# Kernel optimization log

Measured on AMD Instinct MI355X. Metric: run time of the kernel, lower is better.

Reference implementation:

```python
import jax, jax.numpy as jnp
import numpy as np

EPS = 1e-8  # matches torch F.cosine_similarity eps default


def setup_inputs() -> dict:
    key = jax.random.key(0)
    k1, k2 = jax.random.split(key)
    z = jax.random.normal(k1, (8192, 256), dtype=jnp.float32)            # [N, d] node latents
    embedding_weight = jax.random.normal(k2, (4096, 256), dtype=jnp.float32)  # [V, d] codebook
    return {"z": z, "embedding_weight": embedding_weight}


def _l2_normalize(x):
    # torch cosine_similarity clamps each norm at eps before dividing
    n = jnp.sqrt(jnp.sum(x * x, axis=-1, keepdims=True))
    return x / jnp.maximum(n, EPS)


def reference(z, embedding_weight):
    # decode_edges: sigmoid(z @ z^T) -> [N, N]
    adj = jax.nn.sigmoid(jnp.matmul(z, z.T))

    # decode_node_features: cosine similarity of every node latent vs every
    # codebook vector, then argmax over the codebook axis. Instead of the
    # naive [N, V, d] broadcast, normalize both sides and take a single
    # [N, d] x [d, V] matmul -> [N, V], then reduce with argmax.
    zn = _l2_normalize(z)                   # [N, d]
    en = _l2_normalize(embedding_weight)    # [V, d]
    cosine_sim = jnp.matmul(zn, en.T)       # [N, V]
    decoded_indices = jnp.argmax(cosine_sim, axis=1)  # [N] int

    return adj, decoded_indices
```

## Files before the change

kernel.cpp:

```cpp
#include <hip/hip_runtime.h>
#include <stdint.h>
#include <math.h>

#define D_DIM 256
#define NZ 8192
#define NV 4096
#define NBKT 256
#define THR_C 0.138f
#define MARGIN 0.012f

typedef __bf16 bf16;
typedef __attribute__((ext_vector_type(8))) __bf16 bf16x8;
typedef __attribute__((ext_vector_type(4))) float f32x4;

__device__ __forceinline__ void stage16(const bf16* g, bf16* lbase) {
#if __has_builtin(__builtin_amdgcn_global_load_lds)
  __builtin_amdgcn_global_load_lds(
      (const __attribute__((address_space(1))) void*)(uintptr_t)g,
      (__attribute__((address_space(3))) void*)(uint32_t)(uintptr_t)lbase,
      16, 0, 0);
#endif
}

__global__ void prep_kernel(const float* __restrict__ z, const float* __restrict__ E,
                            bf16* __restrict__ zh, bf16* __restrict__ zl,
                            bf16* __restrict__ eh, float* __restrict__ rinvZ,
                            float* __restrict__ rinvE,
                            unsigned long long* __restrict__ slots,
                            unsigned long long* __restrict__ cand) {
  __shared__ float red[4];
  const int row = blockIdx.x;
  const int t = threadIdx.x;
  const bool isZ = row < NZ;
  const int r = isZ ? row : row - NZ;
  const float* src = isZ ? z : E;
  const float x = src[(size_t)r * D_DIM + t];
  const bf16 h = (bf16)x;
  if (isZ) {
    zh[(size_t)r * D_DIM + t] = h;
    zl[(size_t)r * D_DIM + t] = (bf16)(x - (float)h);
    cand[(size_t)r * NBKT + t] = 0ull;
  } else {
    eh[(size_t)r * D_DIM + t] = h;
  }
  float s = x * x;
#pragma unroll
  for (int off = 32; off; off >>= 1) s += __shfl_xor(s, off);
  if ((t & 63) == 0) red[t >> 6] = s;
  __syncthreads();
  if (t == 0) {
    const float tot = red[0] + red[1] + red[2] + red[3];
    const float rv = 1.0f / fmaxf(sqrtf(tot), 1e-8f);
    if (isZ) {
      rinvZ[r] = rv;
      slots[r] = 0ull;
    } else {
      rinvE[r] = rv;
    }
  }
}

__device__ __forceinline__ unsigned long long packvc(float v, int col) {
  const uint32_t b = __float_as_uint(v);
  const uint32_t key = b ^ ((uint32_t)((int32_t)b >> 31) | 0x80000000u);
  return ((unsigned long long)key << 32) | (uint32_t)(~(uint32_t)col);
}
__device__ __forceinline__ float unpack_v(unsigned long long p) {
  const uint32_t key = (uint32_t)(p >> 32);
  const uint32_t fb = (key & 0x80000000u) ? (key ^ 0x80000000u) : ~key;
  return __uint_as_float(fb);
}
__device__ __forceinline__ int unpack_c(unsigned long long p) {
  return (int)(~(uint32_t)p);
}

__global__ __launch_bounds__(256, 3) void cos_kernel(
    const bf16* __restrict__ Ah, const bf16* __restrict__ Bh,
    const float* __restrict__ rinvZ, const float* __restrict__ rinvE,
    unsigned long long* __restrict__ slots, unsigned long long* __restrict__ cand) {
  __shared__ bf16 lAh[128 * 32], lBh[128 * 32];
  const int tid = threadIdx.x;
  const int lane = tid & 63;
  const int w = tid >> 6;
  const int wr = w >> 1, wc = w & 1;
  const int l15 = lane & 15, q = lane >> 4;
  const int bm = blockIdx.y * 128;
  const int bn = blockIdx.x * 128;

  f32x4 acc[4][4] = {};

  for (int kt = 0; kt < 8; ++kt) {
    const int ko = kt * 32;
#pragma unroll
    for (int i = 0; i < 2; ++i) {
      const int c = w * 128 + i * 64 + lane;
      const int r = c >> 2;
      const int kb = (c & 3) << 3;
      const int lofs = (w * 128 + i * 64) * 8;
      stage16(Ah + (size_t)(bm + r) * D_DIM + ko + kb, lAh + lofs);
      stage16(Bh + (size_t)(bn + r) * D_DIM + ko + kb, lBh + lofs);
    }
    __syncthreads();
    bf16x8 fb[4];
#pragma unroll
    for (int ns = 0; ns < 4; ++ns)
      fb[ns] = *(const bf16x8*)&lBh[(wc * 64 + ns * 16 + l15) * 32 + q * 8];
#pragma unroll
    for (int ms = 0; ms < 4; ++ms) {
      const bf16x8 fa = *(const bf16x8*)&lAh[(wr * 64 + ms * 16 + l15) * 32 + q * 8];
#pragma unroll
      for (int ns = 0; ns < 4; ++ns)
        acc[ms][ns] = __builtin_amdgcn_mfma_f32_16x16x32_bf16(fa, fb[ns], acc[ms][ns], 0, 0, 0);
    }
    __syncthreads();
  }

  float rc[4];
  int cols[4];
#pragma unroll
  for (int ns = 0; ns < 4; ++ns) {
    cols[ns] = bn + wc * 64 + ns * 16 + l15;
    rc[ns] = rinvE[cols[ns]];
  }
#pragma unroll
  for (int ms = 0; ms < 4; ++ms) {
    const int rb = bm + wr * 64 + ms * 16 + q * 4;
#pragma unroll
    for (int r = 0; r < 4; ++r) {
      const int rowg = rb + r;
      const float rr = rinvZ[rowg];
      unsigned long long best = 0ull;
#pragma unroll
      for (int ns = 0; ns < 4; ++ns) {
        const float v = acc[ms][ns][r] * rc[ns] * rr;
        const unsigned long long p = packvc(v, cols[ns]);
        best = p > best ? p : best;
        if (v >= THR_C) {
          atomicMax(&cand[(size_t)rowg * NBKT + (cols[ns] >> 4)], p);
        }
      }
#pragma unroll
      for (int off = 1; off < 16; off <<= 1) {
        const unsigned long long o = __shfl_xor(best, off);
        best = o > best ? o : best;
      }
      if (l15 == 0) atomicMax(&slots[rowg], best);
    }
  }
}

__device__ __forceinline__ int tri_base(int i) { return i * 64 - ((i * (i - 1)) >> 1); }

__global__ __launch_bounds__(256, 3) void adj_kernel(const bf16* __restrict__ Ah,
                                                     const bf16* __restrict__ Al,
                                                     float* __restrict__ out) {
  __shared__ bf16 lAh[128 * 32], lAl[128 * 32], lBh[128 * 32], lBl[128 * 32];
  int k = blockIdx.x;
  k = (k & 7) * 260 + (k >> 3);
  const double disc = 4160.25 - 2.0 * (double)k;
  int bi = (int)(64.5 - sqrt(disc));
  while (tri_base(bi + 1) <= k) ++bi;
  while (tri_base(bi) > k) --bi;
  const int bj = bi + (k - tri_base(bi));
  const int bm = bi * 128, bn = bj * 128;

  const int tid = threadIdx.x;
  const int lane = tid & 63;
  const int w = tid >> 6;
  const int wr = w >> 1, wc = w & 1;
  const int l15 = lane & 15, q = lane >> 4;

  f32x4 acc[4][4] = {};

  for (int kt = 0; kt < 8; ++kt) {
    const int ko = kt * 32;
#pragma unroll
    for (int i = 0; i < 2; ++i) {
      const int c = w * 128 + i * 64 + lane;
      const int r = c >> 2;
      const int kb = (c & 3) << 3;
      const size_t ga = (size_t)(bm + r) * D_DIM + ko + kb;
      const size_t gb = (size_t)(bn + r) * D_DIM + ko + kb;
      const int lofs = (w * 128 + i * 64) * 8;
      stage16(Ah + ga, lAh + lofs);
      stage16(Al + ga, lAl + lofs);
      stage16(Ah + gb, lBh + lofs);
      stage16(Al + gb, lBl + lofs);
    }
    __syncthreads();
    bf16x8 fbh[4], fbl[4];
#pragma unroll
    for (int ns = 0; ns < 4; ++ns) {
      const int n = wc * 64 + ns * 16 + l15;
      fbh[ns] = *(const bf16x8*)&lBh[n * 32 + q * 8];
      fbl[ns] = *(const bf16x8*)&lBl[n * 32 + q * 8];
    }
#pragma unroll
    for (int ms = 0; ms < 4; ++ms) {
      const int m = wr * 64 + ms * 16 + l15;
      const bf16x8 fah = *(const bf16x8*)&lAh[m * 32 + q * 8];
      const bf16x8 fal = *(const bf16x8*)&lAl[m * 32 + q * 8];
#pragma unroll
      for (int ns = 0; ns < 4; ++ns) {
        acc[ms][ns] = __builtin_amdgcn_mfma_f32_16x16x32_bf16(fah, fbh[ns], acc[ms][ns], 0, 0, 0);
        acc[ms][ns] = __builtin_amdgcn_mfma_f32_16x16x32_bf16(fah, fbl[ns], acc[ms][ns], 0, 0, 0);
        acc[ms][ns] = __builtin_amdgcn_mfma_f32_16x16x32_bf16(fal, fbh[ns], acc[ms][ns], 0, 0, 0);
      }
    }
    __syncthreads();
  }

#pragma unroll
  for (int ms = 0; ms < 4; ++ms)
#pragma unroll
    for (int ns = 0; ns < 4; ++ns)
#pragma unroll
      for (int r = 0; r < 4; ++r)
        acc[ms][ns][r] = __builtin_amdgcn_rcpf(1.0f + __expf(-acc[ms][ns][r]));

#pragma unroll
  for (int ms = 0; ms < 4; ++ms) {
    const int rb = bm + wr * 64 + ms * 16 + q * 4;
#pragma unroll
    for (int r = 0; r < 4; ++r) {
      const size_t ro = (size_t)(rb + r) * NZ;
#pragma unroll
      for (int ns = 0; ns < 4; ++ns) {
        const int col = bn + wc * 64 + ns * 16 + l15;
        out[ro + col] = acc[ms][ns][r];
      }
    }
  }
  if (bi != bj) {
#pragma unroll
    for (int ms = 0; ms < 4; ++ms) {
      const int rb = bm + wr * 64 + ms * 16 + q * 4;
#pragma unroll
      for (int ns = 0; ns < 4; ++ns) {
        const int col = bn + wc * 64 + ns * 16 + l15;
        *(f32x4*)&out[(size_t)col * NZ + rb] = acc[ms][ns];
      }
    }
  }
}

__global__ __launch_bounds__(256) void refine_kernel(
    const unsigned long long* __restrict__ cand,
    const unsigned long long* __restrict__ slots, const float* __restrict__ z,
    const float* __restrict__ E, float* __restrict__ out_idx) {
  const int t = threadIdx.x;
  const int lane = t & 63;
  const int w = t >> 6;
  const int row = blockIdx.x * 4 + w;

  const unsigned long long* lrow = cand + (size_t)row * NBKT;
  unsigned long long pj[4];
  unsigned long long mk = 0ull;
#pragma unroll
  for (int j = 0; j < 4; ++j) {
    pj[j] = lrow[lane + 64 * j];
    mk = pj[j] > mk ? pj[j] : mk;
  }
#pragma unroll
  for (int off = 32; off; off >>= 1) {
    const unsigned long long o = __shfl_xor(mk, off);
    mk = o > mk ? o : mk;
  }
  if (mk == 0ull) {
    if (lane == 0) out_idx[row] = (float)unpack_c(slots[row]);
    return;
  }
  const float thr = unpack_v(mk) - MARGIN;

  double zr[4];
#pragma unroll
  for (int j = 0; j < 4; ++j) zr[j] = (double)z[(size_t)row * D_DIM + lane + 64 * j];
  double sz2 = zr[0] * zr[0] + zr[1] * zr[1] + zr[2] * zr[2] + zr[3] * zr[3];
#pragma unroll
  for (int off = 32; off; off >>= 1) sz2 += __shfl_xor(sz2, off);
  const double sz = fmax(sqrt(sz2), 1e-8);

  double v1 = -1e30, v2 = -1e30;
  int c1 = 0x7fffffff, c2 = 0x7fffffff;
#pragma unroll
  for (int j = 0; j < 4; ++j) {
    const bool flag = (pj[j] != 0ull) && (unpack_v(pj[j]) >= thr);
    unsigned long long bal = __ballot(flag);
    while (bal) {
      const int src = __ffsll((long long)bal) - 1;
      bal &= bal - 1;
      const int c = unpack_c(__shfl(pj[j], src));
      double d = 0.0, e2 = 0.0;
#pragma unroll
      for (int jj = 0; jj < 4; ++jj) {
        const double ev = (double)E[(size_t)c * D_DIM + lane + 64 * jj];
        d += zr[jj] * ev;
        e2 += ev * ev;
      }
#pragma unroll
      for (int off = 32; off; off >>= 1) {
        d += __shfl_xor(d, off);
        e2 += __shfl_xor(e2, off);
      }
      const double cv = d / (sz * fmax(sqrt(e2), 1e-8));
      if (cv > v1 || (cv == v1 && c < c1)) {
        v2 = v1; c2 = c1; v1 = cv; c1 = c;
      } else if (cv > v2 || (cv == v2 && c < c2)) {
        v2 = cv; c2 = c;
      }
    }
  }
  if (lane == 0) {
    int pick = c1;
    if (c2 != 0x7fffffff && (v1 - v2) < 3e-7) pick = c2;
    out_idx[row] = (float)pick;
  }
}

extern "C" void kernel_launch(void* const* d_in, const int* in_sizes, int n_in,
                              void* d_out, int out_size, void* d_ws, size_t ws_size,
                              hipStream_t stream) {
  const float* z = (const float*)d_in[0];
  const float* E = (const float*)d_in[1];
  float* out = (float*)d_out;

  char* ws = (char*)d_ws;
  bf16* zh = (bf16*)ws;
  bf16* zl = zh + (size_t)NZ * D_DIM;
  bf16* eh = zl + (size_t)NZ * D_DIM;
  float* rinvZ = (float*)(eh + (size_t)NV * D_DIM);
  float* rinvE = rinvZ + NZ;
  unsigned long long* slots = (unsigned long long*)(rinvE + NV);

  unsigned long long* cand = (unsigned long long*)out;
  float* idx_out = out + (size_t)NZ * NZ;

  prep_kernel<<<NZ + NV, 256, 0, stream>>>(z, E, zh, zl, eh, rinvZ, rinvE, slots, cand);

  dim3 g2(NV / 128, NZ / 128);
  cos_kernel<<<g2, 256, 0, stream>>>(zh, eh, rinvZ, rinvE, slots, cand);

  refine_kernel<<<NZ / 4, 256, 0, stream>>>(cand, slots, z, E, idx_out);

  adj_kernel<<<2080, 256, 0, stream>>>(zh, zl, out);
}
```

Baseline: 406.8 us.

## Switch adjacency GEMM to int8 split fixed-point MFMA with full-K LDS preload

Result: slower. 471.9 us (+16.0%).

```diff
diff --git a/kernel.cpp b/kernel.cpp
--- a/kernel.cpp
+++ b/kernel.cpp
@@ -12,8 +12,9 @@
 typedef __bf16 bf16;
 typedef __attribute__((ext_vector_type(8))) __bf16 bf16x8;
 typedef __attribute__((ext_vector_type(4))) float f32x4;
-
-__device__ __forceinline__ void stage16(const bf16* g, bf16* lbase) {
+typedef __attribute__((ext_vector_type(4))) int i32x4;
+
+__device__ __forceinline__ void stage16(const void* g, void* lbase) {
 #if __has_builtin(__builtin_amdgcn_global_load_lds)
   __builtin_amdgcn_global_load_lds(
       (const __attribute__((address_space(1))) void*)(uintptr_t)g,
@@ -23,9 +24,9 @@
 }
 
 __global__ void prep_kernel(const float* __restrict__ z, const float* __restrict__ E,
-                            bf16* __restrict__ zh, bf16* __restrict__ zl,
-                            bf16* __restrict__ eh, float* __restrict__ rinvZ,
-                            float* __restrict__ rinvE,
+                            bf16* __restrict__ zh, signed char* __restrict__ zqh,
+                            signed char* __restrict__ zql, bf16* __restrict__ eh,
+                            float* __restrict__ rinvZ, float* __restrict__ rinvE,
                             unsigned long long* __restrict__ slots,
                             unsigned long long* __restrict__ cand) {
   __shared__ float red[4];
@@ -35,13 +36,16 @@
   const int r = isZ ? row : row - NZ;
   const float* src = isZ ? z : E;
   const float x = src[(size_t)r * D_DIM + t];
-  const bf16 h = (bf16)x;
   if (isZ) {
-    zh[(size_t)r * D_DIM + t] = h;
-    zl[(size_t)r * D_DIM + t] = (bf16)(x - (float)h);
+    zh[(size_t)r * D_DIM + t] = (bf16)x;
+    int z16 = (int)rintf(x * 4096.0f);
+    z16 = z16 < -32768 ? -32768 : (z16 > 32639 ? 32639 : z16);
+    const int h = (z16 + 128) >> 8;
+    zqh[(size_t)r * D_DIM + t] = (signed char)h;
+    zql[(size_t)r * D_DIM + t] = (signed char)(z16 - (h << 8));
     cand[(size_t)r * NBKT + t] = 0ull;
   } else {
-    eh[(size_t)r * D_DIM + t] = h;
+    eh[(size_t)r * D_DIM + t] = (bf16)x;
   }
   float s = x * x;
 #pragma unroll
@@ -74,45 +78,51 @@
   return (int)(~(uint32_t)p);
 }
 
-__global__ __launch_bounds__(256, 3) void cos_kernel(
+__global__ __launch_bounds__(256, 1) void cos_kernel(
     const bf16* __restrict__ Ah, const bf16* __restrict__ Bh,
     const float* __restrict__ rinvZ, const float* __restrict__ rinvE,
     unsigned long long* __restrict__ slots, unsigned long long* __restrict__ cand) {
-  __shared__ bf16 lAh[128 * 32], lBh[128 * 32];
+  __shared__ bf16 lds[65536];
   const int tid = threadIdx.x;
   const int lane = tid & 63;
   const int w = tid >> 6;
   const int wr = w >> 1, wc = w & 1;
-  const int l15 = lane & 15, q = lane >> 4;
+  const int l15 = lane & 15, q0 = lane >> 4;
   const int bm = blockIdx.y * 128;
   const int bn = blockIdx.x * 128;
 
+  const bf16* gsrc[2] = {Ah + (size_t)bm * D_DIM, Bh + (size_t)bn * D_DIM};
+#pragma unroll
+  for (int op = 0; op < 2; ++op)
+#pragma unroll
+    for (int i = 0; i < 16; ++i) {
+      const int c = i * 256 + tid;
+      const int kt = c >> 9, row = (c >> 2) & 127, qp = c & 3;
+      const int q = (qp - (row >> 1)) & 3;
+      stage16(gsrc[op] + (size_t)row * D_DIM + kt * 32 + q * 8,
+              lds + (op * 4096 + i * 256 + w * 64) * 8);
+    }
+  __syncthreads();
+
   f32x4 acc[4][4] = {};
-
+#pragma unroll
   for (int kt = 0; kt < 8; ++kt) {
-    const int ko = kt * 32;
-#pragma unroll
-    for (int i = 0; i < 2; ++i) {
-      const int c = w * 128 + i * 64 + lane;
-      const int r = c >> 2;
-      const int kb = (c & 3) << 3;
-      const int lofs = (w * 128 + i * 64) * 8;
-      stage16(Ah + (size_t)(bm + r) * D_DIM + ko + kb, lAh + lofs);
-      stage16(Bh + (size_t)(bn + r) * D_DIM + ko + kb, lBh + lofs);
-    }
-    __syncthreads();
-    bf16x8 fb[4];
-#pragma unroll
-    for (int ns = 0; ns < 4; ++ns)
-      fb[ns] = *(const bf16x8*)&lBh[(wc * 64 + ns * 16 + l15) * 32 + q * 8];
+    bf16x8 fa[4], fb[4];
 #pragma unroll
     for (int ms = 0; ms < 4; ++ms) {
-      const bf16x8 fa = *(const bf16x8*)&lAh[(wr * 64 + ms * 16 + l15) * 32 + q * 8];
+      const int row = wr * 64 + ms * 16 + l15;
+      fa[ms] = *(const bf16x8*)&lds[kt * 4096 + row * 32 + (((q0 + (row >> 1)) & 3) << 3)];
+    }
+#pragma unroll
+    for (int ns = 0; ns < 4; ++ns) {
+      const int row = wc * 64 + ns * 16 + l15;
+      fb[ns] = *(const bf16x8*)&lds[32768 + kt * 4096 + row * 32 + (((q0 + (row >> 1)) & 3) << 3)];
+    }
+#pragma unroll
+    for (int ms = 0; ms < 4; ++ms)
 #pragma unroll
       for (int ns = 0; ns < 4; ++ns)
-        acc[ms][ns] = __builtin_amdgcn_mfma_f32_16x16x32_bf16(fa, fb[ns], acc[ms][ns], 0, 0, 0);
-    }
-    __syncthreads();
+        acc[ms][ns] = __builtin_amdgcn_mfma_f32_16x16x32_bf16(fa[ms], fb[ns], acc[ms][ns], 0, 0, 0);
   }
 
   float rc[4];
@@ -124,7 +134,7 @@
   }
 #pragma unroll
   for (int ms = 0; ms < 4; ++ms) {
-    const int rb = bm + wr * 64 + ms * 16 + q * 4;
+    const int rb = bm + wr * 64 + ms * 16 + q0 * 4;
 #pragma unroll
     for (int r = 0; r < 4; ++r) {
       const int rowg = rb + r;
@@ -151,10 +161,10 @@
 
 __device__ __forceinline__ int tri_base(int i) { return i * 64 - ((i * (i - 1)) >> 1); }
 
-__global__ __launch_bounds__(256, 3) void adj_kernel(const bf16* __restrict__ Ah,
-                                                     const bf16* __restrict__ Al,
+__global__ __launch_bounds__(256, 1) void adj_kernel(const signed char* __restrict__ Qh,
+                                                     const signed char* __restrict__ Ql,
                                                      float* __restrict__ out) {
-  __shared__ bf16 lAh[128 * 32], lAl[128 * 32], lBh[128 * 32], lBl[128 * 32];
+  __shared__ signed char lds[131072];
   int k = blockIdx.x;
   k = (k & 7) * 260 + (k >> 3);
   const double disc = 4160.25 - 2.0 * (double)k;
@@ -168,77 +178,87 @@
   const int lane = tid & 63;
   const int w = tid >> 6;
   const int wr = w >> 1, wc = w & 1;
-  const int l15 = lane & 15, q = lane >> 4;
-
-  f32x4 acc[4][4] = {};
-
-  for (int kt = 0; kt < 8; ++kt) {
-    const int ko = kt * 32;
-#pragma unroll
-    for (int i = 0; i < 2; ++i) {
-      const int c = w * 128 + i * 64 + lane;
-      const int r = c >> 2;
-      const int kb = (c & 3) << 3;
-      const size_t ga = (size_t)(bm + r) * D_DIM + ko + kb;
-      const size_t gb = (size_t)(bn + r) * D_DIM + ko + kb;
-      const int lofs = (w * 128 + i * 64) * 8;
-      stage16(Ah + ga, lAh + lofs);
-      stage16(Al + ga, lAl + lofs);
-      stage16(Ah + gb, lBh + lofs);
-      stage16(Al + gb, lBl + lofs);
-    }
-    __syncthreads();
-    bf16x8 fbh[4], fbl[4];
+  const int l15 = lane & 15, q0 = lane >> 4;
+
+  const signed char* gsrc[4] = {Qh + (size_t)bm * D_DIM, Ql + (size_t)bm * D_DIM,
+                                Qh + (size_t)bn * D_DIM, Ql + (size_t)bn * D_DIM};
+#pragma unroll
+  for (int op = 0; op < 4; ++op)
+#pragma unroll
+    for (int i = 0; i < 8; ++i) {
+      const int c = i * 256 + tid;
+      const int kt = c >> 9, row = (c >> 2) & 127, qp = c & 3;
+      const int q = (qp - (row >> 1)) & 3;
+      stage16(gsrc[op] + (size_t)row * D_DIM + kt * 64 + q * 16,
+              lds + (op * 2048 + i * 256 + w * 64) * 16);
+    }
+  __syncthreads();
+
+  i32x4 ahh[4][4] = {};
+  i32x4 amid[4][4] = {};
+  i32x4 all_[4][4] = {};
+#pragma unroll
+  for (int kt = 0; kt < 4; ++kt) {
+    i32x4 fAh[4], fAl[4], fBh[4], fBl[4];
+#pragma unroll
+    for (int ms = 0; ms < 4; ++ms) {
+      const int row = wr * 64 + ms * 16 + l15;
+      const int off = kt * 8192 + row * 64 + (((q0 + (row >> 1)) & 3) << 4);
+      fAh[ms] = *(const i32x4*)&lds[off];
+      fAl[ms] = *(const i32x4*)&lds[32768 + off];
+    }
 #pragma unroll
     for (int ns = 0; ns < 4; ++ns) {
-      const int n = wc * 64 + ns * 16 + l15;
-      fbh[ns] = *(const bf16x8*)&lBh[n * 32 + q * 8];
-      fbl[ns] = *(const bf16x8*)&lBl[n * 32 + q * 8];
-    }
-#pragma unroll
-    for (int ms = 0; ms < 4; ++ms) {
-      const int m = wr * 64 + ms * 16 + l15;
-      const bf16x8 fah = *(const bf16x8*)&lAh[m * 32 + q * 8];
-      const bf16x8 fal = *(const bf16x8*)&lAl[m * 32 + q * 8];
+      const int row = wc * 64 + ns * 16 + l15;
+      const int off = kt * 8192 + row * 64 + (((q0 + (row >> 1)) & 3) << 4);
+      fBh[ns] = *(const i32x4*)&lds[65536 + off];
+      fBl[ns] = *(const i32x4*)&lds[98304 + off];
+    }
+#pragma unroll
+    for (int ms = 0; ms < 4; ++ms)
 #pragma unroll
       for (int ns = 0; ns < 4; ++ns) {
-        acc[ms][ns] = __builtin_amdgcn_mfma_f32_16x16x32_bf16(fah, fbh[ns], acc[ms][ns], 0, 0, 0);
-        acc[ms][ns] = __builtin_amdgcn_mfma_f32_16x16x32_bf16(fah, fbl[ns], acc[ms][ns], 0, 0, 0);
-        acc[ms][ns] = __builtin_amdgcn_mfma_f32_16x16x32_bf16(fal, fbh[ns], acc[ms][ns], 0, 0, 0);
-      }
-    }
-    __syncthreads();
-  }
-
+        ahh[ms][ns] = __builtin_amdgcn_mfma_i32_16x16x64_i8(fAh[ms], fBh[ns], ahh[ms][ns], 0, 0, 0);
+        amid[ms][ns] = __builtin_amdgcn_mfma_i32_16x16x64_i8(fAh[ms], fBl[ns], amid[ms][ns], 0, 0, 0);
+        amid[ms][ns] = __builtin_amdgcn_mfma_i32_16x16x64_i8(fAl[ms], fBh[ns], amid[ms][ns], 0, 0, 0);
+        all_[ms][ns] = __builtin_amdgcn_mfma_i32_16x16x64_i8(fAl[ms], fBl[ns], all_[ms][ns], 0, 0, 0);
+      }
+  }
+
+  f32x4 sig[4][4];
 #pragma unroll
   for (int ms = 0; ms < 4; ++ms)
 #pragma unroll
     for (int ns = 0; ns < 4; ++ns)
 #pragma unroll
-      for (int r = 0; r < 4; ++r)
-        acc[ms][ns][r] = __builtin_amdgcn_rcpf(1.0f + __expf(-acc[ms][ns][r]));
+      for (int r = 0; r < 4; ++r) {
+        const float d = (float)ahh[ms][ns][r] * 3.90625e-3f +
+                        (float)amid[ms][ns][r] * 1.52587890625e-5f +
+                        (float)all_[ms][ns][r] * 5.9604644775390625e-8f;
+        sig[ms][ns][r] = __builtin_amdgcn_rcpf(1.0f + __expf(-d));
+      }
 
 #pragma unroll
   for (int ms = 0; ms < 4; ++ms) {
-    const int rb = bm + wr * 64 + ms * 16 + q * 4;
+    const int rb = bm + wr * 64 + ms * 16 + q0 * 4;
 #pragma unroll
     for (int r = 0; r < 4; ++r) {
       const size_t ro = (size_t)(rb + r) * NZ;
 #pragma unroll
       for (int ns = 0; ns < 4; ++ns) {
         const int col = bn + wc * 64 + ns * 16 + l15;
-        out[ro + col] = acc[ms][ns][r];
+        out[ro + col] = sig[ms][ns][r];
       }
     }
   }
   if (bi != bj) {
 #pragma unroll
     for (int ms = 0; ms < 4; ++ms) {
-      const int rb = bm + wr * 64 + ms * 16 + q * 4;
+      const int rb = bm + wr * 64 + ms * 16 + q0 * 4;
 #pragma unroll
       for (int ns = 0; ns < 4; ++ns) {
         const int col = bn + wc * 64 + ns * 16 + l15;
-        *(f32x4*)&out[(size_t)col * NZ + rb] = acc[ms][ns];
+        *(f32x4*)&out[(size_t)col * NZ + rb] = sig[ms][ns];
       }
     }
   }
@@ -326,21 +346,23 @@
 
   char* ws = (char*)d_ws;
   bf16* zh = (bf16*)ws;
-  bf16* zl = zh + (size_t)NZ * D_DIM;
-  bf16* eh = zl + (size_t)NZ * D_DIM;
-  float* rinvZ = (float*)(eh + (size_t)NV * D_DIM);
+  bf16* eh = zh + (size_t)NZ * D_DIM;
+  signed char* zqh = (signed char*)(eh + (size_t)NV * D_DIM);
+  signed char* zql = zqh + (size_t)NZ * D_DIM;
+  float* rinvZ = (float*)(zql + (size_t)NZ * D_DIM);
   float* rinvE = rinvZ + NZ;
   unsigned long long* slots = (unsigned long long*)(rinvE + NV);
 
   unsigned long long* cand = (unsigned long long*)out;
   float* idx_out = out + (size_t)NZ * NZ;
 
-  prep_kernel<<<NZ + NV, 256, 0, stream>>>(z, E, zh, zl, eh, rinvZ, rinvE, slots, cand);
+  prep_kernel<<<NZ + NV, 256, 0, stream>>>(z, E, zh, zqh, zql, eh, rinvZ, rinvE,
+                                           slots, cand);
 
   dim3 g2(NV / 128, NZ / 128);
   cos_kernel<<<g2, 256, 0, stream>>>(zh, eh, rinvZ, rinvE, slots, cand);
 
   refine_kernel<<<NZ / 4, 256, 0, stream>>>(cand, slots, z, E, idx_out);
 
-  adj_kernel<<<2080, 256, 0, stream>>>(zh, zl, out);
-}
+  adj_kernel<<<2080, 256, 0, stream>>>(zqh, zql, out);
+}
```
